# Kernel tuning notes

Measured on AMD Instinct MI355X. Metric: run time of the kernel, lower is better.

## Reference

```python
import jax, jax.numpy as jnp
from jax import lax
import numpy as np

N, C, H, W = 16, 128, 128, 128
CH = C // 4  # adapter contraction channels


def setup_inputs() -> dict:
    key = jax.random.key(0)
    ks = jax.random.split(key, 12)
    x = jax.random.normal(ks[0], (N, C, H, W), jnp.float32)
    # intensity in {1,2,3} as the torch module expects (intensity[i]-1 indexes adapters)
    intensity = jax.random.randint(ks[1], (N,), 1, 4)
    conv1_w = jax.random.normal(ks[2], (C, C, 3, 3), jnp.float32) * 0.02
    conv1_b = jnp.zeros((C,), jnp.float32)
    prelu1 = jnp.float32(0.25)  # nn.PReLU default single shared slope
    conv2_w = jax.random.normal(ks[3], (C, C, 3, 3), jnp.float32) * 0.02
    conv2_b = jnp.zeros((C,), jnp.float32)
    # 3 adapter experts, stacked on leading axis
    aW1 = jax.random.normal(ks[4], (3, CH, C), jnp.float32) * 0.05
    ab1 = jnp.zeros((3, CH), jnp.float32)
    aW2 = jax.random.normal(ks[5], (3, C, CH), jnp.float32) * 0.05
    ab2 = jnp.zeros((3, C), jnp.float32)
    prelu2 = jnp.float32(0.25)
    return dict(x=x, intensity=intensity, conv1_w=conv1_w, conv1_b=conv1_b,
                prelu1=prelu1, conv2_w=conv2_w, conv2_b=conv2_b,
                aW1=aW1, ab1=ab1, aW2=aW2, ab2=ab2, prelu2=prelu2)


def prelu(x, a):
    return jnp.where(x >= 0, x, a * x)


def conv3x3(x, w, b):
    y = lax.conv_general_dilated(x, w, window_strides=(1, 1),
                                 padding=((1, 1), (1, 1)),
                                 dimension_numbers=('NCHW', 'OIHW', 'NCHW'))
    return y + b[None, :, None, None]


def reference(x, intensity, conv1_w, conv1_b, prelu1, conv2_w, conv2_b,
              aW1, ab1, aW2, ab2, prelu2):
    h = prelu(conv3x3(x, conv1_w, conv1_b), prelu1)      # conv1 + PReLU
    h = conv3x3(h, conv2_w, conv2_b)                     # conv2, no activation
    x1 = jnp.mean(h, axis=(2, 3))                        # AdaptiveAvgPool2d(1)+Flatten -> [N,C]
    idx = intensity - 1                                  # expert id per sample
    W1, b1 = aW1[idx], ab1[idx]                          # gather per-sample expert weights
    W2, b2 = aW2[idx], ab2[idx]
    a = jax.nn.relu(jnp.einsum('nc,nhc->nh', x1, W1) + b1)
    g = jnp.einsum('nh,nch->nc', a, W2) + b2             # [N,C]
    out = h * jax.nn.sigmoid(g)[:, :, None, None] + x    # gated residual
    return prelu(out, prelu2)
```

## Files before the change

### kernel.cpp

```cpp
#include <hip/hip_runtime.h>
#include <hip/hip_bf16.h>
#include <math.h>

#define NN   16
#define C_   128
#define HH   128
#define WW   128
#define CHID 32
#define NTILES 64

typedef short bf16x8 __attribute__((ext_vector_type(8)));
typedef float f32x4  __attribute__((ext_vector_type(4)));

__device__ inline void glds16(const void* g, void* l) {
    __builtin_amdgcn_global_load_lds(
        (const __attribute__((address_space(1))) unsigned int*)g,
        (__attribute__((address_space(3))) unsigned int*)l, 16, 0, 0);
}

__device__ inline unsigned short f2bf(float f) {
    __hip_bfloat16 h = __float2bfloat16(f);
    return *reinterpret_cast<unsigned short*>(&h);
}

__global__ __launch_bounds__(64) void pack_w_k(
    const float* __restrict__ w1, const float* __restrict__ w2,
    unsigned short* __restrict__ wl)
{
    const int b = blockIdx.x;
    const int conv = b / 288, rem = b % 288;
    const int kk = rem / 32, ck = (rem % 32) / 8, cot = rem % 8;
    const int l = threadIdx.x;
    const int co  = cot * 16 + (l & 15);
    const int ci0 = ck * 32 + (l >> 4) * 8;
    const float* W = conv ? w2 : w1;
    union { unsigned short u[8]; uint4 v; } pk;
#pragma unroll
    for (int j = 0; j < 8; ++j)
        pk.u[j] = f2bf(W[(size_t)(co * C_ + ci0 + j) * 9 + kk]);
    unsigned short* dst = wl + (size_t)conv * 147456 +
        ((((size_t)kk * 4 + ck) * 8 + cot) * 64 + l) * 8;
    *reinterpret_cast<uint4*>(dst) = pk.v;
}

__global__ __launch_bounds__(256) void to_cnhwc_k(
    const float* __restrict__ x, unsigned short* __restrict__ xb)
{
    __shared__ unsigned short s_t[128][136];
    const int y = blockIdx.x, n = blockIdx.y, t = threadIdx.x;

#pragma unroll
    for (int p = 0; p < 16; ++p) {
        int fi = p * 256 + t;
        int ci = fi >> 5, x0 = (fi & 31) * 4;
        float4 v = *reinterpret_cast<const float4*>(
            x + (((size_t)(n * C_ + ci) * HH) + y) * WW + x0);
        const int slot = ((ci >> 3) ^ ((x0 >> 2) & 7)) * 8 + (ci & 7);
        s_t[x0 + 0][slot] = f2bf(v.x);
        s_t[x0 + 1][slot] = f2bf(v.y);
        s_t[x0 + 2][slot] = f2bf(v.z);
        s_t[x0 + 3][slot] = f2bf(v.w);
    }
    __syncthreads();
    unsigned short* dstbase = xb + ((size_t)(n * HH + y)) * 16384;
#pragma unroll
    for (int p = 0; p < 8; ++p) {
        int o = p * 256 + t;
        int sl = o >> 8, u = o & 255;
        int xc = u >> 1, q = u & 1;
        int oct = sl * 2 + q;
        uint4 v = *reinterpret_cast<const uint4*>(
            &s_t[xc][(oct ^ ((xc >> 2) & 7)) * 8]);
        *reinterpret_cast<uint4*>(dstbase + (size_t)sl * 2048 + xc * 16 + q * 8) = v;
    }
}

template<int MODE>
__global__ __launch_bounds__(512) void conv_mfma_k(
    const unsigned short* __restrict__ inb,
    const unsigned short* __restrict__ wl,
    const float* __restrict__ bias,
    const float* __restrict__ prelu_a,
    unsigned short* __restrict__ outb,
    float* __restrict__ outf,
    float* __restrict__ partial)
{
    __shared__ char  smem[34816];
    __shared__ float s_part[8][64];

    const int tid = threadIdx.x;
    const int l = tid & 63, w = tid >> 6;
    const int wco = w >> 2, wy = (w >> 1) & 1, wxh = w & 1;
    const int lg = l >> 4, l15 = l & 15;
    const int yp = blockIdx.x, n = blockIdx.z;
    const int y0 = yp * 2;
    const int rot = (yp + n) & 3;

    const f32x4 fz = {0.f, 0.f, 0.f, 0.f};
    f32x4 acc[4][4];
#pragma unroll
    for (int m = 0; m < 4; ++m)
#pragma unroll
        for (int nf = 0; nf < 4; ++nf) acc[m][nf] = fz;

    const bf16x8* wv = reinterpret_cast<const bf16x8*>(wl);
    char* sb = smem;
    const uint4 z4 = {0u, 0u, 0u, 0u};

    auto stage = [&](int ck) {
        const int r = w >> 1, xh = w & 1;
        const int ygl = y0 - 1 + r;
        if (ygl < 0 || ygl >= HH) {
            int t2 = xh * 64 + l;
            for (int i = t2; i < 528; i += 128)
                *reinterpret_cast<uint4*>(sb + r * 8448 + i * 16) = z4;
        } else {
            if (xh == 0 && l < 8) {
                int col = (l < 4) ? 0 : 129, q = l & 3;
                *reinterpret_cast<uint4*>(sb + r * 8448 + col * 64 + q * 16) = z4;
            }
            const size_t rowbase = ((size_t)(n * HH + ygl)) * 32768;
#pragma unroll
            for (int i = 0; i < 4; ++i) {
                const int p  = xh * 64 + i * 16 + (l >> 2);
                const int sd = (l & 3) ^ (((1 + p) >> 1) & 3);
                const char* g = (const char*)inb + rowbase +
                    (size_t)(2 * ck + (sd >> 1)) * 4096 + p * 32 + (sd & 1) * 16;
                glds16(g, sb + r * 8448 + (1 + xh * 64 + i * 16) * 64);
            }
        }
    };

    for (int c8 = 0; c8 < 4; ++c8) {
        const int ck = (c8 + rot) & 3;
        __syncthreads();
        stage(ck);
        __syncthreads();

        bf16x8 a_cur[4];
#pragma unroll
        for (int m = 0; m < 4; ++m)
            a_cur[m] = wv[(((size_t)0 * 4 + ck) * 8 + wco * 4 + m) * 64 + l];

#pragma unroll
        for (int kk = 0; kk < 9; ++kk) {
            const int ky = kk / 3, kx = kk % 3;
            bf16x8 a_nxt[4];
            if (kk < 8) {
#pragma unroll
                for (int m = 0; m < 4; ++m)
                    a_nxt[m] = wv[((((size_t)kk + 1) * 4 + ck) * 8 + wco * 4 + m) * 64 + l];
            }
            const int rrow = wy + ky;
            bf16x8 b[4];
#pragma unroll
            for (int nf = 0; nf < 4; ++nf) {
                int xi = wxh * 64 + nf * 16 + l15 + kx;
                int slot = lg ^ ((xi >> 1) & 3);
                b[nf] = *reinterpret_cast<const bf16x8*>(
                    sb + rrow * 8448 + xi * 64 + slot * 16);
            }
#pragma unroll
            for (int nf = 0; nf < 4; ++nf)
#pragma unroll
                for (int m = 0; m < 4; ++m)
                    acc[m][nf] = __builtin_amdgcn_mfma_f32_16x16x32_bf16(
                        a_cur[m], b[nf], acc[m][nf], 0, 0, 0);
            if (kk < 8) {
#pragma unroll
                for (int m = 0; m < 4; ++m) a_cur[m] = a_nxt[m];
            }
        }
    }
    __syncthreads();

    const int ybase = y0 + wy;
    if (MODE == 0 || MODE == 1) {
        const float a1 = (MODE == 0) ? *prelu_a : 0.f;
        float ps[4][4];
        if (MODE == 1) {
#pragma unroll
            for (int m = 0; m < 4; ++m)
#pragma unroll
                for (int jj = 0; jj < 4; ++jj) ps[m][jj] = 0.f;
        }
        unsigned short (*s_rp)[136] = reinterpret_cast<unsigned short (*)[136]>(smem);
        for (int r = 0; r < 2; ++r) {
            if (wy == r) {
#pragma unroll
                for (int m = 0; m < 4; ++m) {
                    const int co0 = wco * 64 + m * 16 + lg * 4;
#pragma unroll
                    for (int nf = 0; nf < 4; ++nf) {
                        const int xc = wxh * 64 + nf * 16 + l15;
                        union { unsigned short u[4]; uint2 v; } pk;
#pragma unroll
                        for (int jj = 0; jj < 4; ++jj) {
                            float f = acc[m][nf][jj] + bias[co0 + jj];
                            if (MODE == 0) f = (f >= 0.f) ? f : a1 * f;
                            else           ps[m][jj] += f;
                            pk.u[jj] = f2bf(f);
                        }
                        *reinterpret_cast<uint2*>(&s_rp[xc][co0]) = pk.v;
                    }
                }
            }
            __syncthreads();
            const int y = y0 + r;
#pragma unroll
            for (int p = 0; p < 4; ++p) {
                int u = p * 512 + tid;
                int xc = u >> 4, k = u & 15;
                uint4 v = *reinterpret_cast<const uint4*>(&s_rp[xc][k * 8]);
                *reinterpret_cast<uint4*>(outb +
                    (((size_t)(n * HH + y)) * 8 + (k >> 1)) * 2048 +
                    xc * 16 + (k & 1) * 8) = v;
            }
            __syncthreads();
        }
        if (MODE == 1) {
#pragma unroll
            for (int m = 0; m < 4; ++m)
#pragma unroll
                for (int jj = 0; jj < 4; ++jj) {
                    float s = ps[m][jj];
                    s += __shfl_xor(s, 1); s += __shfl_xor(s, 2);
                    s += __shfl_xor(s, 4); s += __shfl_xor(s, 8);
                    ps[m][jj] = s;
                }
            if (l15 == 0) {
#pragma unroll
                for (int m = 0; m < 4; ++m)
#pragma unroll
                    for (int jj = 0; jj < 4; ++jj)
                        s_part[w][m * 16 + lg * 4 + jj] = ps[m][jj];
            }
            __syncthreads();
            if (tid < C_) {
                const int half = tid >> 6;
                float s = 0.f;
#pragma unroll
                for (int w2 = 0; w2 < 4; ++w2) s += s_part[half * 4 + w2][tid & 63];
                partial[((size_t)(n * C_ + tid)) * NTILES + yp] = s;
            }
        }
    } else {
        float ps[4][4];
#pragma unroll
        for (int m = 0; m < 4; ++m)
#pragma unroll
            for (int jj = 0; jj < 4; ++jj) ps[m][jj] = 0.f;
#pragma unroll
        for (int m = 0; m < 4; ++m) {
            const int co0 = wco * 64 + m * 16 + lg * 4;
#pragma unroll
            for (int nf = 0; nf < 4; ++nf) {
                const int xc = wxh * 64 + nf * 16 + l15;
#pragma unroll
                for (int jj = 0; jj < 4; ++jj) {
                    float f = acc[m][nf][jj] + bias[co0 + jj];
                    outf[(((size_t)(n * C_ + co0 + jj)) * HH + ybase) * WW + xc] = f;
                    ps[m][jj] += f;
                }
            }
        }
#pragma unroll
        for (int m = 0; m < 4; ++m)
#pragma unroll
            for (int jj = 0; jj < 4; ++jj) {
                float s = ps[m][jj];
                s += __shfl_xor(s, 1); s += __shfl_xor(s, 2);
                s += __shfl_xor(s, 4); s += __shfl_xor(s, 8);
                ps[m][jj] = s;
            }
        if (l15 == 0) {
#pragma unroll
            for (int m = 0; m < 4; ++m)
#pragma unroll
                for (int jj = 0; jj < 4; ++jj)
                    s_part[w][m * 16 + lg * 4 + jj] = ps[m][jj];
        }
        __syncthreads();
        if (tid < C_) {
            const int half = tid >> 6;
            float s = 0.f;
#pragma unroll
            for (int w2 = 0; w2 < 4; ++w2) s += s_part[half * 4 + w2][tid & 63];
            partial[((size_t)(n * C_ + tid)) * NTILES + yp] = s;
        }
    }
}

__global__ __launch_bounds__(C_) void adapter_k(
    const float* __restrict__ partial, const int* __restrict__ intensity,
    const float* __restrict__ aW1, const float* __restrict__ ab1,
    const float* __restrict__ aW2, const float* __restrict__ ab2,
    float* __restrict__ sig)
{
    __shared__ float sx[C_];
    __shared__ float sa[CHID];
    const int n = blockIdx.x, c = threadIdx.x;

    float s = 0.f;
    for (int t = 0; t < NTILES; ++t)
        s += partial[(size_t)(n * C_ + c) * NTILES + t];
    sx[c] = s * (1.f / (float)(HH * WW));
    __syncthreads();

    const int idx = intensity[n] - 1;
    if (c < CHID) {
        float a = ab1[idx * CHID + c];
        const float* wrow = aW1 + (size_t)(idx * CHID + c) * C_;
        for (int k = 0; k < C_; ++k) a = fmaf(wrow[k], sx[k], a);
        sa[c] = fmaxf(a, 0.f);
    }
    __syncthreads();

    float g = ab2[idx * C_ + c];
    const float* w2row = aW2 + (size_t)(idx * C_ + c) * CHID;
#pragma unroll
    for (int k = 0; k < CHID; ++k) g = fmaf(w2row[k], sa[k], g);
    sig[n * C_ + c] = 1.f / (1.f + expf(-g));
}

__global__ __launch_bounds__(256) void epilogue_bf16_k(
    const unsigned short* __restrict__ h2b, const float* __restrict__ x,
    const float* __restrict__ sig, const float* __restrict__ prelu_a,
    float* __restrict__ out)
{
    __shared__ unsigned short s_h[128][136];
    const int y = blockIdx.x, n = blockIdx.y, t = threadIdx.x;
    const float a = *prelu_a;
    const unsigned short* slab = h2b + ((size_t)(n * HH + y)) * 16384;

#pragma unroll
    for (int p = 0; p < 8; ++p) {
        int o = p * 256 + t;
        int sl = o >> 8, u = o & 255;
        int xc = u >> 1, q = u & 1;
        int oct = sl * 2 + q;
        uint4 v = *reinterpret_cast<const uint4*>(
            slab + (size_t)sl * 2048 + xc * 16 + q * 8);
        *reinterpret_cast<uint4*>(&s_h[xc][(oct ^ ((xc >> 2) & 7)) * 8]) = v;
    }
    __syncthreads();

#pragma unroll
    for (int p = 0; p < 16; ++p) {
        int fi = p * 256 + t;
        int ci = fi >> 5, x0 = (fi & 31) * 4;
        const float sg = sig[n * C_ + ci];
        float4 x4 = *reinterpret_cast<const float4*>(
            x + (((size_t)(n * C_ + ci)) * HH + y) * WW + x0);
        float4 v;
        float hv[4];
#pragma unroll
        for (int j = 0; j < 4; ++j) {
            int xr = x0 + j;
            unsigned short hu = s_h[xr][((ci >> 3) ^ ((xr >> 2) & 7)) * 8 + (ci & 7)];
            unsigned int bits = ((unsigned int)hu) << 16;
            hv[j] = *reinterpret_cast<float*>(&bits);
        }
        v.x = hv[0] * sg + x4.x;  v.x = (v.x >= 0.f) ? v.x : a * v.x;
        v.y = hv[1] * sg + x4.y;  v.y = (v.y >= 0.f) ? v.y : a * v.y;
        v.z = hv[2] * sg + x4.z;  v.z = (v.z >= 0.f) ? v.z : a * v.z;
        v.w = hv[3] * sg + x4.w;  v.w = (v.w >= 0.f) ? v.w : a * v.w;
        *reinterpret_cast<float4*>(
            out + (((size_t)(n * C_ + ci)) * HH + y) * WW + x0) = v;
    }
}

__global__ __launch_bounds__(256) void epilogue_k(
    const float* __restrict__ x, const float* __restrict__ sig,
    const float* __restrict__ prelu_a, float* __restrict__ out, int total4)
{
    const float a = *prelu_a;
    const int stride = gridDim.x * blockDim.x;
    for (int i = blockIdx.x * blockDim.x + threadIdx.x; i < total4; i += stride) {
        const int nc = (i * 4) >> 14;
        const float s = sig[nc];
        float4 h4 = ((const float4*)out)[i];
        float4 x4 = ((const float4*)x)[i];
        float4 v;
        v.x = h4.x * s + x4.x;  v.x = (v.x >= 0.f) ? v.x : a * v.x;
        v.y = h4.y * s + x4.y;  v.y = (v.y >= 0.f) ? v.y : a * v.y;
        v.z = h4.z * s + x4.z;  v.z = (v.z >= 0.f) ? v.z : a * v.z;
        v.w = h4.w * s + x4.w;  v.w = (v.w >= 0.f) ? v.w : a * v.w;
        ((float4*)out)[i] = v;
    }
}

extern "C" void kernel_launch(void* const* d_in, const int* in_sizes, int n_in,
                              void* d_out, int out_size, void* d_ws, size_t ws_size,
                              hipStream_t stream)
{
    const float* x         = (const float*)d_in[0];
    const int*   intensity = (const int*)  d_in[1];
    const float* w1        = (const float*)d_in[2];
    const float* b1        = (const float*)d_in[3];
    const float* p1        = (const float*)d_in[4];
    const float* w2        = (const float*)d_in[5];
    const float* b2        = (const float*)d_in[6];
    const float* aW1       = (const float*)d_in[7];
    const float* ab1       = (const float*)d_in[8];
    const float* aW2       = (const float*)d_in[9];
    const float* ab2       = (const float*)d_in[10];
    const float* p2        = (const float*)d_in[11];
    float* out = (float*)d_out;

    const size_t SLAB = (size_t)33554432 * 2;
    const size_t WLB  = (size_t)294912 * 2;
    const size_t NEED = 2 * SLAB + WLB + (size_t)(NN * C_ * NTILES + NN * C_ + 64) * 4;
    const bool big = ws_size >= NEED;

    unsigned short* h1b = (unsigned short*)d_ws;
    unsigned short* xb;
    unsigned short* h2b = nullptr;
    unsigned short* wl;
    if (big) {
        xb  = (unsigned short*)((char*)d_ws + SLAB);
        h2b = xb;
        wl  = (unsigned short*)((char*)d_ws + 2 * SLAB);
    } else {
        xb  = (unsigned short*)d_out;
        wl  = (unsigned short*)((char*)d_ws + SLAB);
    }
    float* partial = (float*)((char*)wl + WLB);
    float* sig     = partial + (size_t)NN * C_ * NTILES;

    pack_w_k<<<dim3(576), dim3(64), 0, stream>>>(w1, w2, wl);
    to_cnhwc_k<<<dim3(HH, NN), dim3(256), 0, stream>>>(x, xb);

    conv_mfma_k<0><<<dim3(NTILES, 1, NN), dim3(512), 0, stream>>>(
        xb, wl, b1, p1, h1b, nullptr, nullptr);

    if (big) {
        conv_mfma_k<1><<<dim3(NTILES, 1, NN), dim3(512), 0, stream>>>(
            h1b, wl + (size_t)147456, b2, nullptr, h2b, nullptr, partial);
        adapter_k<<<dim3(NN), dim3(C_), 0, stream>>>(
            partial, intensity, aW1, ab1, aW2, ab2, sig);
        epilogue_bf16_k<<<dim3(HH, NN), dim3(256), 0, stream>>>(
            h2b, x, sig, p2, out);
    } else {
        conv_mfma_k<2><<<dim3(NTILES, 1, NN), dim3(512), 0, stream>>>(
            h1b, wl + (size_t)147456, b2, nullptr, nullptr, out, partial);
        adapter_k<<<dim3(NN), dim3(C_), 0, stream>>>(
            partial, intensity, aW1, ab1, aW2, ab2, sig);
        const int total4 = NN * C_ * HH * WW / 4;
        epilogue_k<<<dim3(2048), dim3(256), 0, stream>>>(x, sig, p2, out, total4);
    }
}
```

Baseline: 262.0 us.

## Double-buffer LDS input staging and deepen weight/B prefetch in conv MFMA loop

The input tile in LDS is now double-buffered, so the global-to-LDS load for the next channel chunk is issued before the MFMA loop on the current chunk, and one barrier per chunk is removed. Weight fragments are prefetched two taps ahead and LDS B fragments one tap ahead, using rotating register arrays. The aim is to hide global and LDS latency behind MFMA work. In exchange, LDS use roughly doubles to about 68KB per block and register pressure rises, which may reduce occupancy.

```diff
diff --git a/kernel.cpp b/kernel.cpp
--- a/kernel.cpp
+++ b/kernel.cpp
@@ -8,6 +8,8 @@
 #define WW   128
 #define CHID 32
 #define NTILES 64
+
+#define BCHUNK 33792
 
 typedef short bf16x8 __attribute__((ext_vector_type(8)));
 typedef float f32x4  __attribute__((ext_vector_type(4)));
@@ -85,7 +87,7 @@
     float* __restrict__ outf,
     float* __restrict__ partial)
 {
-    __shared__ char  smem[34816];
+    __shared__ char  smem[2 * BCHUNK];
     __shared__ float s_part[8][64];
 
     const int tid = threadIdx.x;
@@ -104,10 +106,9 @@
         for (int nf = 0; nf < 4; ++nf) acc[m][nf] = fz;
 
     const bf16x8* wv = reinterpret_cast<const bf16x8*>(wl);
-    char* sb = smem;
     const uint4 z4 = {0u, 0u, 0u, 0u};
 
-    auto stage = [&](int ck) {
+    auto stage = [&](int ck, char* sb) {
         const int r = w >> 1, xh = w & 1;
         const int ygl = y0 - 1 + r;
         if (ygl < 0 || ygl >= HH) {
@@ -131,48 +132,50 @@
         }
     };
 
+    stage(rot, smem);
+    __syncthreads();
+
     for (int c8 = 0; c8 < 4; ++c8) {
         const int ck = (c8 + rot) & 3;
-        __syncthreads();
-        stage(ck);
-        __syncthreads();
-
-        bf16x8 a_cur[4];
-#pragma unroll
-        for (int m = 0; m < 4; ++m)
-            a_cur[m] = wv[(((size_t)0 * 4 + ck) * 8 + wco * 4 + m) * 64 + l];
-
-#pragma unroll
-        for (int kk = 0; kk < 9; ++kk) {
+        char* buf = smem + (c8 & 1) * BCHUNK;
+        if (c8 < 3) stage((c8 + 1 + rot) & 3, smem + ((c8 + 1) & 1) * BCHUNK);
+
+        auto loadA = [&](int kk, bf16x8* a) {
+#pragma unroll
+            for (int m = 0; m < 4; ++m)
+                a[m] = wv[(((size_t)kk * 4 + ck) * 8 + wco * 4 + m) * 64 + l];
+        };
+        auto rdB = [&](int kk, bf16x8* b) {
             const int ky = kk / 3, kx = kk % 3;
-            bf16x8 a_nxt[4];
-            if (kk < 8) {
-#pragma unroll
-                for (int m = 0; m < 4; ++m)
-                    a_nxt[m] = wv[((((size_t)kk + 1) * 4 + ck) * 8 + wco * 4 + m) * 64 + l];
-            }
             const int rrow = wy + ky;
-            bf16x8 b[4];
 #pragma unroll
             for (int nf = 0; nf < 4; ++nf) {
                 int xi = wxh * 64 + nf * 16 + l15 + kx;
                 int slot = lg ^ ((xi >> 1) & 3);
                 b[nf] = *reinterpret_cast<const bf16x8*>(
-                    sb + rrow * 8448 + xi * 64 + slot * 16);
-            }
+                    buf + rrow * 8448 + xi * 64 + slot * 16);
+            }
+        };
+
+        bf16x8 ap[3][4], bp[2][4];
+        loadA(0, ap[0]);
+        loadA(1, ap[1]);
+        rdB(0, bp[0]);
+#pragma unroll
+        for (int kk = 0; kk < 9; ++kk) {
+            if (kk < 7) loadA(kk + 2, ap[(kk + 2) % 3]);
+            if (kk < 8) rdB(kk + 1, bp[(kk + 1) & 1]);
+            bf16x8* ac = ap[kk % 3];
+            bf16x8* bc = bp[kk & 1];
 #pragma unroll
             for (int nf = 0; nf < 4; ++nf)
 #pragma unroll
                 for (int m = 0; m < 4; ++m)
                     acc[m][nf] = __builtin_amdgcn_mfma_f32_16x16x32_bf16(
-                        a_cur[m], b[nf], acc[m][nf], 0, 0, 0);
-            if (kk < 8) {
-#pragma unroll
-                for (int m = 0; m < 4; ++m) a_cur[m] = a_nxt[m];
-            }
-        }
-    }
-    __syncthreads();
+                        ac[m], bc[nf], acc[m][nf], 0, 0, 0);
+        }
+        __syncthreads();
+    }
 
     const int ybase = y0 + wy;
     if (MODE == 0 || MODE == 1) {
```

New measurement: 272.1 us. +3.9%, slower.

## Double-buffer conv input staging and enlarge tile to four output rows

Applied to the files above, without the earlier changes.

The conv kernel now computes four output rows per block instead of two, with each wave covering a full 128-wide row (8 N-fragments). The halo input rows per channel chunk are staged into one of two LDS buffers while MFMA work runs on the other, which removes one barrier per chunk and overlaps the global-to-LDS loads with compute. Each block reads 6 input rows for 4 output rows instead of 4 for 2, so halo refetch drops. In exchange, LDS use grows to about 100KB per block and accumulator registers double, which may lower occupancy or cause spills.

```diff
diff --git a/kernel.cpp b/kernel.cpp
--- a/kernel.cpp
+++ b/kernel.cpp
@@ -7,7 +7,10 @@
 #define HH   128
 #define WW   128
 #define CHID 32
-#define NTILES 64
+#define NTILES 32
+
+#define ROWB  8448
+#define BUFB  50688
 
 typedef short bf16x8 __attribute__((ext_vector_type(8)));
 typedef float f32x4  __attribute__((ext_vector_type(4)));
@@ -85,57 +88,58 @@
     float* __restrict__ outf,
     float* __restrict__ partial)
 {
-    __shared__ char  smem[34816];
+    __shared__ char  smem[2 * BUFB];
     __shared__ float s_part[8][64];
 
     const int tid = threadIdx.x;
     const int l = tid & 63, w = tid >> 6;
-    const int wco = w >> 2, wy = (w >> 1) & 1, wxh = w & 1;
+    const int wco = w >> 2, wy = w & 3;
     const int lg = l >> 4, l15 = l & 15;
-    const int yp = blockIdx.x, n = blockIdx.z;
-    const int y0 = yp * 2;
-    const int rot = (yp + n) & 3;
+    const int yg = blockIdx.x, n = blockIdx.z;
+    const int y0 = yg * 4;
+    const int rot = (yg + n) & 3;
 
     const f32x4 fz = {0.f, 0.f, 0.f, 0.f};
-    f32x4 acc[4][4];
+    f32x4 acc[4][8];
 #pragma unroll
     for (int m = 0; m < 4; ++m)
 #pragma unroll
-        for (int nf = 0; nf < 4; ++nf) acc[m][nf] = fz;
+        for (int nf = 0; nf < 8; ++nf) acc[m][nf] = fz;
 
     const bf16x8* wv = reinterpret_cast<const bf16x8*>(wl);
-    char* sb = smem;
     const uint4 z4 = {0u, 0u, 0u, 0u};
 
-    auto stage = [&](int ck) {
-        const int r = w >> 1, xh = w & 1;
-        const int ygl = y0 - 1 + r;
-        if (ygl < 0 || ygl >= HH) {
-            int t2 = xh * 64 + l;
-            for (int i = t2; i < 528; i += 128)
-                *reinterpret_cast<uint4*>(sb + r * 8448 + i * 16) = z4;
-        } else {
-            if (xh == 0 && l < 8) {
-                int col = (l < 4) ? 0 : 129, q = l & 3;
-                *reinterpret_cast<uint4*>(sb + r * 8448 + col * 64 + q * 16) = z4;
-            }
-            const size_t rowbase = ((size_t)(n * HH + ygl)) * 32768;
-#pragma unroll
-            for (int i = 0; i < 4; ++i) {
-                const int p  = xh * 64 + i * 16 + (l >> 2);
+    auto stage = [&](int ck, char* sb) {
+        if (tid < 48) {
+            const int r = tid >> 3, col = ((tid >> 2) & 1) ? 129 : 0, q = tid & 3;
+            *reinterpret_cast<uint4*>(sb + r * ROWB + col * 64 + q * 16) = z4;
+        }
+#pragma unroll
+        for (int i = 0; i < 6; ++i) {
+            const int g   = w + i * 8;
+            const int row = g >> 3, seg = g & 7;
+            const int ygl = y0 - 1 + row;
+            char* dst = sb + row * ROWB + (1 + seg * 16) * 64;
+            if (ygl < 0 || ygl >= HH) {
+                *reinterpret_cast<uint4*>(dst + l * 16) = z4;
+            } else {
+                const int p  = seg * 16 + (l >> 2);
                 const int sd = (l & 3) ^ (((1 + p) >> 1) & 3);
-                const char* g = (const char*)inb + rowbase +
+                const char* g_src = (const char*)inb +
+                    ((size_t)(n * HH + ygl)) * 32768 +
                     (size_t)(2 * ck + (sd >> 1)) * 4096 + p * 32 + (sd & 1) * 16;
-                glds16(g, sb + r * 8448 + (1 + xh * 64 + i * 16) * 64);
+                glds16(g_src, dst);
             }
         }
     };
+
+    stage(rot, smem);
+    __syncthreads();
 
     for (int c8 = 0; c8 < 4; ++c8) {
         const int ck = (c8 + rot) & 3;
-        __syncthreads();
-        stage(ck);
-        __syncthreads();
+        char* buf = smem + (c8 & 1) * BUFB;
+        if (c8 < 3) stage((c8 + 1 + rot) & 3, smem + ((c8 + 1) & 1) * BUFB);
 
         bf16x8 a_cur[4];
 #pragma unroll
@@ -152,16 +156,16 @@
                     a_nxt[m] = wv[((((size_t)kk + 1) * 4 + ck) * 8 + wco * 4 + m) * 64 + l];
             }
             const int rrow = wy + ky;
-            bf16x8 b[4];
-#pragma unroll
-            for (int nf = 0; nf < 4; ++nf) {
-                int xi = wxh * 64 + nf * 16 + l15 + kx;
+            bf16x8 b[8];
+#pragma unroll
+            for (int nf = 0; nf < 8; ++nf) {
+                int xi = nf * 16 + l15 + kx;
                 int slot = lg ^ ((xi >> 1) & 3);
                 b[nf] = *reinterpret_cast<const bf16x8*>(
-                    sb + rrow * 8448 + xi * 64 + slot * 16);
-            }
-#pragma unroll
-            for (int nf = 0; nf < 4; ++nf)
+                    buf + rrow * ROWB + xi * 64 + slot * 16);
+            }
+#pragma unroll
+            for (int nf = 0; nf < 8; ++nf)
 #pragma unroll
                 for (int m = 0; m < 4; ++m)
                     acc[m][nf] = __builtin_amdgcn_mfma_f32_16x16x32_bf16(
@@ -171,10 +175,9 @@
                 for (int m = 0; m < 4; ++m) a_cur[m] = a_nxt[m];
             }
         }
-    }
-    __syncthreads();
-
-    const int ybase = y0 + wy;
+        __syncthreads();
+    }
+
     if (MODE == 0 || MODE == 1) {
         const float a1 = (MODE == 0) ? *prelu_a : 0.f;
         float ps[4][4];
@@ -185,14 +188,14 @@
                 for (int jj = 0; jj < 4; ++jj) ps[m][jj] = 0.f;
         }
         unsigned short (*s_rp)[136] = reinterpret_cast<unsigned short (*)[136]>(smem);
-        for (int r = 0; r < 2; ++r) {
+        for (int r = 0; r < 4; ++r) {
             if (wy == r) {
 #pragma unroll
                 for (int m = 0; m < 4; ++m) {
                     const int co0 = wco * 64 + m * 16 + lg * 4;
 #pragma unroll
-                    for (int nf = 0; nf < 4; ++nf) {
-                        const int xc = wxh * 64 + nf * 16 + l15;
+                    for (int nf = 0; nf < 8; ++nf) {
+                        const int xc = nf * 16 + l15;
                         union { unsigned short u[4]; uint2 v; } pk;
 #pragma unroll
                         for (int jj = 0; jj < 4; ++jj) {
@@ -241,10 +244,11 @@
                 float s = 0.f;
 #pragma unroll
                 for (int w2 = 0; w2 < 4; ++w2) s += s_part[half * 4 + w2][tid & 63];
-                partial[((size_t)(n * C_ + tid)) * NTILES + yp] = s;
+                partial[((size_t)(n * C_ + tid)) * NTILES + yg] = s;
             }
         }
     } else {
+        const int ybase = y0 + wy;
         float ps[4][4];
 #pragma unroll
         for (int m = 0; m < 4; ++m)
@@ -254,8 +258,8 @@
         for (int m = 0; m < 4; ++m) {
             const int co0 = wco * 64 + m * 16 + lg * 4;
 #pragma unroll
-            for (int nf = 0; nf < 4; ++nf) {
-                const int xc = wxh * 64 + nf * 16 + l15;
+            for (int nf = 0; nf < 8; ++nf) {
+                const int xc = nf * 16 + l15;
 #pragma unroll
                 for (int jj = 0; jj < 4; ++jj) {
                     float f = acc[m][nf][jj] + bias[co0 + jj];
@@ -286,7 +290,7 @@
             float s = 0.f;
 #pragma unroll
             for (int w2 = 0; w2 < 4; ++w2) s += s_part[half * 4 + w2][tid & 63];
-            partial[((size_t)(n * C_ + tid)) * NTILES + yp] = s;
+            partial[((size_t)(n * C_ + tid)) * NTILES + yg] = s;
         }
     }
 }
```

Measured after the change: 258.2 us. Within noise of the previous version (-1.5%).
